# Kernel optimization log

Measured on AMD Instinct MI355X. Metric: run time of the kernel, lower is better.

Reference implementation:

```python
import jax, jax.numpy as jnp
import numpy as np

TEMPERATURE = 0.1
SIGMA = 1.0
NUM_CLASSES = 4
INF = 1e8
EPS = 1e-12


def _l2_normalize(x):
    n = jnp.sqrt(jnp.sum(x * x, axis=-1, keepdims=True))
    return x / jnp.maximum(n, EPS)


def _rbf_kernel(y, gamma):
    # y: [M, P] -> [M, M] exp(-gamma * ||yi - yj||^2)
    sq = jnp.sum(y * y, axis=-1)
    d2 = sq[:, None] + sq[None, :] - 2.0 * (y @ y.T)
    d2 = jnp.maximum(d2, 0.0)
    return jnp.exp(-gamma * d2)


def setup_inputs() -> dict:
    key = jax.random.key(0)
    k1, k2, k3, k4 = jax.random.split(key, 4)
    N, D = 2048, 512
    return {
        "z_i": jax.random.normal(k1, (N, D), dtype=jnp.float32),
        "z_j": jax.random.normal(k2, (N, D), dtype=jnp.float32),
        "labels": jax.random.randint(k3, (N,), 0, NUM_CLASSES, dtype=jnp.int64),
        "z_pos": jax.random.uniform(k4, (N, 1), dtype=jnp.float32),
    }


def reference(z_i, z_j, labels, z_pos):
    N = z_i.shape[0]
    zi = _l2_normalize(z_i)
    zj = _l2_normalize(z_j)

    eye_n = jnp.eye(N, dtype=zi.dtype)
    sim_zii = (zi @ zi.T) / TEMPERATURE - INF * eye_n
    sim_zjj = (zj @ zj.T) / TEMPERATURE - INF * eye_n
    sim_zij = (zi @ zj.T) / TEMPERATURE

    # label agreement mask over the 2N x 2N augmented batch
    labs = jax.nn.one_hot(labels, NUM_CLASSES, dtype=jnp.float32)
    L = jnp.concatenate([labs, labs], axis=0)          # [2N, C]
    eye_2n = jnp.eye(2 * N, dtype=jnp.float32)
    mask = (L @ L.T) * (1.0 - eye_2n)

    # RBF kernel weights over positional labels (detached in original)
    all_pos = jnp.tile(z_pos.reshape(N, -1), (2, 1))   # [2N, P]
    gamma = 1.0 / (2.0 * SIGMA ** 2)
    weights = _rbf_kernel(all_pos, gamma) * (1.0 - eye_2n)

    final_weights = weights * mask
    # NB: torch broadcasting divides column j by rowsum[j]; matrix is symmetric
    final_weights = final_weights / final_weights.sum(axis=1)

    top = jnp.concatenate([sim_zii, sim_zij], axis=1)
    bot = jnp.concatenate([sim_zij.T, sim_zjj], axis=1)
    sim_Z = jnp.concatenate([top, bot], axis=0)        # [2N, 2N]

    log_sim_Z = jax.nn.log_softmax(sim_Z, axis=1)
    loss = (-1.0 / N) * jnp.sum(log_sim_Z * final_weights)
    return loss
```

## Files before the change

kernel.cpp:

```cpp
#include <hip/hip_runtime.h>
#include <hip/hip_bf16.h>

#define D 512
#define INV_T 10.0f
#define INF_VAL 1e8f

#define BM 128
#define BN 128
#define BK 64
#define KSTEPS (D / BK)
#define NTB 32
#define NBLK (NTB * (NTB + 1) / 2)
#define NCHUNK 64

typedef short bf16x8 __attribute__((ext_vector_type(8)));
typedef float f32x4 __attribute__((ext_vector_type(4)));

typedef __attribute__((address_space(3))) unsigned int lds_uint;
typedef __attribute__((address_space(1))) unsigned int gbl_uint;

__device__ __forceinline__ void async_copy16(const ushort* gsrc, ushort* ldst) {
  __builtin_amdgcn_global_load_lds((const gbl_uint*)gsrc, (lds_uint*)ldst, 16, 0, 0);
}

__device__ inline float wave_reduce_sum(float v) {
#pragma unroll
  for (int off = 32; off > 0; off >>= 1) v += __shfl_xor(v, off);
  return v;
}

__device__ __forceinline__ ushort f2bf(float x) {
  __hip_bfloat16 h = __float2bfloat16(x);
  return *reinterpret_cast<ushort*>(&h);
}

__global__ __launch_bounds__(256) void k_prep(const float* __restrict__ zi,
                                              const float* __restrict__ zj,
                                              ushort* __restrict__ zb,
                                              const int* __restrict__ labels,
                                              const float* __restrict__ zpos,
                                              float* __restrict__ sinv, int N) {
  int b = blockIdx.x;
  if (b < 1024) {
    int wv = threadIdx.x >> 6, lane = threadIdx.x & 63;
    int row = b * 4 + wv;
    const float* src = (row < N) ? (zi + (size_t)row * D) : (zj + (size_t)(row - N) * D);
    const float4* s4 = reinterpret_cast<const float4*>(src);
    float4 v0 = s4[lane];
    float4 v1 = s4[lane + 64];
    float ss = 0.f;
    ss = fmaf(v0.x, v0.x, ss); ss = fmaf(v0.y, v0.y, ss);
    ss = fmaf(v0.z, v0.z, ss); ss = fmaf(v0.w, v0.w, ss);
    ss = fmaf(v1.x, v1.x, ss); ss = fmaf(v1.y, v1.y, ss);
    ss = fmaf(v1.z, v1.z, ss); ss = fmaf(v1.w, v1.w, ss);
    ss = wave_reduce_sum(ss);
    float sc = 1.0f / fmaxf(sqrtf(ss), 1e-12f);
    ushort4 o0 = {f2bf(v0.x * sc), f2bf(v0.y * sc), f2bf(v0.z * sc), f2bf(v0.w * sc)};
    ushort4 o1 = {f2bf(v1.x * sc), f2bf(v1.y * sc), f2bf(v1.z * sc), f2bf(v1.w * sc)};
    ushort4* dst = reinterpret_cast<ushort4*>(zb + (size_t)row * D);
    dst[lane] = o0;
    dst[lane + 64] = o1;
  } else {
    __shared__ float scratch[4];
    int j = b - 1024;
    int lj = labels[j];
    float pj = zpos[j];
    float s = 0.f;
    for (int i = threadIdx.x; i < N; i += 256) {
      if (labels[i] == lj) {
        float d = zpos[i] - pj;
        s += __expf(-0.5f * d * d);
      }
    }
    s = wave_reduce_sum(s);
    int lane = threadIdx.x & 63, wv = threadIdx.x >> 6;
    if (lane == 0) scratch[wv] = s;
    __syncthreads();
    if (threadIdx.x == 0) {
      float t = scratch[0] + scratch[1] + scratch[2] + scratch[3];
      sinv[j] = 1.0f / (2.0f * t - 1.0f);
    }
  }
}

__global__ __launch_bounds__(256) void k_tt(const int* __restrict__ labels,
                                            const float* __restrict__ zpos,
                                            const float* __restrict__ sinv,
                                            float* __restrict__ tt, int N) {
  __shared__ float scratch[4];
  int i = blockIdx.x;
  int li = labels[i];
  float pi = zpos[i];
  float s = 0.f;
  for (int j = threadIdx.x; j < N; j += 256) {
    if (labels[j] == li) {
      float d = zpos[j] - pi;
      s += __expf(-0.5f * d * d) * sinv[j];
    }
  }
  s = wave_reduce_sum(s);
  int lane = threadIdx.x & 63, wv = threadIdx.x >> 6;
  if (lane == 0) scratch[wv] = s;
  __syncthreads();
  if (threadIdx.x == 0) {
    tt[i] = scratch[0] + scratch[1] + scratch[2] + scratch[3];
  }
}

__global__ __launch_bounds__(256, 2) void k_gemm(
    const ushort* __restrict__ zb, const int* __restrict__ labels,
    const float* __restrict__ zpos, const float* __restrict__ sinv,
    float* __restrict__ s_ws, float* __restrict__ c_ws, int N) {
  __shared__ __align__(16) ushort sT[2][2][BM * BK];

  const int tid = threadIdx.x;
  const int lane = tid & 63;
  const int wv = tid >> 6;
  const int wr = wv >> 1;
  const int wc = wv & 1;
  const int colq = lane & 15;
  const int laneg = lane >> 4;
  const int twoN = 2 * N;

  const int bid = blockIdx.x;
  int L = (bid & 7) * (NBLK / 8) + (bid >> 3);
  int u = L, rt = 0;
  while (u >= NTB - rt) { u -= NTB - rt; ++rt; }
  const int ct = rt + u;
  const bool diag = (rt == ct);
  const int rowBase = rt * BM;
  const int colBase = ct * BN;

  const int srow = lane >> 3;
  const int sslot = (lane & 7) ^ srow;

  f32x4 acc[4][4] = {};

  {
#pragma unroll
    for (int q = 0; q < 4; ++q) {
      int rloc = wv * 32 + q * 8;
      async_copy16(zb + (size_t)(rowBase + rloc + srow) * D + 0 * BK + sslot * 8,
                   (ushort*)sT[0][0] + rloc * BK);
      if (!diag)
        async_copy16(zb + (size_t)(colBase + rloc + srow) * D + 0 * BK + sslot * 8,
                     (ushort*)sT[0][1] + rloc * BK);
    }
  }
  __syncthreads();

  int cur = 0;
#pragma unroll
  for (int kt = 0; kt < KSTEPS; ++kt) {
    if (kt + 1 < KSTEPS) {
#pragma unroll
      for (int q = 0; q < 4; ++q) {
        int rloc = wv * 32 + q * 8;
        async_copy16(zb + (size_t)(rowBase + rloc + srow) * D + (kt + 1) * BK + sslot * 8,
                     (ushort*)sT[cur ^ 1][0] + rloc * BK);
        if (!diag)
          async_copy16(zb + (size_t)(colBase + rloc + srow) * D + (kt + 1) * BK + sslot * 8,
                       (ushort*)sT[cur ^ 1][1] + rloc * BK);
      }
    }

    const char* Ab = reinterpret_cast<const char*>(sT[cur][0]);
    const char* Bb = diag ? Ab : reinterpret_cast<const char*>(sT[cur][1]);
#pragma unroll
    for (int kk = 0; kk < 2; ++kk) {
      bf16x8 a[4], b[4];
      const int slot = kk * 4 + laneg;
#pragma unroll
      for (int rf = 0; rf < 4; ++rf) {
        int r = wr * 64 + rf * 16 + colq;
        a[rf] = *reinterpret_cast<const bf16x8*>(Ab + r * 128 + (slot ^ (r & 7)) * 16);
      }
#pragma unroll
      for (int cf = 0; cf < 4; ++cf) {
        int c = wc * 64 + cf * 16 + colq;
        b[cf] = *reinterpret_cast<const bf16x8*>(Bb + c * 128 + (slot ^ (c & 7)) * 16);
      }
#pragma unroll
      for (int rf = 0; rf < 4; ++rf)
#pragma unroll
        for (int cf = 0; cf < 4; ++cf)
          acc[rf][cf] = __builtin_amdgcn_mfma_f32_16x16x32_bf16(a[rf], b[cf], acc[rf][cf], 0, 0, 0);
    }

    if (kt + 1 < KSTEPS) {
      __syncthreads();
      cur ^= 1;
    }
  }

  const int wRowBase = rowBase + wr * 64;
  const int wColBase = colBase + wc * 64;
  const int rmodBase = (wRowBase >= N) ? wRowBase - N : wRowBase;
  const int cmodBase = (wColBase >= N) ? wColBase - N : wColBase;

  float rpos[16], rsinv[16];
  unsigned rlab = 0;
#pragma unroll
  for (int rf = 0; rf < 4; ++rf)
#pragma unroll
    for (int rg = 0; rg < 4; ++rg) {
      int idx = rf * 4 + rg;
      int r = rmodBase + rf * 16 + laneg * 4 + rg;
      rpos[idx] = zpos[r];
      rsinv[idx] = sinv[r];
      rlab |= ((unsigned)labels[r] & 3u) << (idx * 2);
    }

  float s_p[16], c_p[16], sc_p[4], cc_p[4];
#pragma unroll
  for (int i = 0; i < 16; ++i) { s_p[i] = 0.f; c_p[i] = 0.f; }

#pragma unroll
  for (int cf = 0; cf < 4; ++cf) {
    int jc = cmodBase + cf * 16 + colq;
    int lc = labels[jc];
    float pc = zpos[jc];
    float si = sinv[jc];
    int col = wColBase + cf * 16 + colq;
    float scf = 0.f, ccf = 0.f;
#pragma unroll
    for (int rf = 0; rf < 4; ++rf)
#pragma unroll
      for (int rg = 0; rg < 4; ++rg) {
        int idx = rf * 4 + rg;
        int row = wRowBase + rf * 16 + laneg * 4 + rg;
        float sim = acc[rf][cf][rg] * INV_T;
        bool dg = (row == col);
        if (dg) sim = -INF_VAL;
        float e = __expf(sim - 10.f);
        s_p[idx] += e;
        scf += e;
        int lr = (int)((rlab >> (idx * 2)) & 3u);
        if (lr == lc && !dg) {
          float d = rpos[idx] - pc;
          float w = __expf(-0.5f * d * d);
          c_p[idx] = fmaf(w * si, sim, c_p[idx]);
          ccf = fmaf(w * rsinv[idx], sim, ccf);
        }
      }
    sc_p[cf] = scf;
    cc_p[cf] = ccf;
  }

#pragma unroll
  for (int idx = 0; idx < 16; ++idx) {
#pragma unroll
    for (int off = 1; off < 16; off <<= 1) {
      s_p[idx] += __shfl_xor(s_p[idx], off);
      c_p[idx] += __shfl_xor(c_p[idx], off);
    }
  }
  if (colq == 0) {
    int cc = ct * 2 + wc;
#pragma unroll
    for (int rf = 0; rf < 4; ++rf)
#pragma unroll
      for (int rg = 0; rg < 4; ++rg) {
        int idx = rf * 4 + rg;
        int row = wRowBase + rf * 16 + laneg * 4 + rg;
        s_ws[(size_t)cc * twoN + row] = s_p[idx];
        c_ws[(size_t)cc * twoN + row] = c_p[idx];
      }
  }

  if (!diag) {
#pragma unroll
    for (int cf = 0; cf < 4; ++cf) {
      sc_p[cf] += __shfl_xor(sc_p[cf], 16);
      sc_p[cf] += __shfl_xor(sc_p[cf], 32);
      cc_p[cf] += __shfl_xor(cc_p[cf], 16);
      cc_p[cf] += __shfl_xor(cc_p[cf], 32);
    }
    if (laneg == 0) {
      int cct = rt * 2 + wr;
#pragma unroll
      for (int cf = 0; cf < 4; ++cf) {
        int rowt = wColBase + cf * 16 + colq;
        s_ws[(size_t)cct * twoN + rowt] = sc_p[cf];
        c_ws[(size_t)cct * twoN + rowt] = cc_p[cf];
      }
    }
  }
}

__global__ __launch_bounds__(256) void k_combine(const float* __restrict__ s_ws,
                                                 const float* __restrict__ c_ws,
                                                 const float* __restrict__ sinv,
                                                 const float* __restrict__ tt,
                                                 float* __restrict__ partial, int N) {
  int a = blockIdx.x * 256 + threadIdx.x;
  int twoN = 2 * N;
  if (a >= twoN) return;
  float s = 0.f, c = 0.f;
  for (int cc = 0; cc < NCHUNK; ++cc) {
    s += s_ws[(size_t)cc * twoN + a];
    c += c_ws[(size_t)cc * twoN + a];
  }
  int ir = (a >= N) ? a - N : a;
  float lse = 10.f + logf(s);
  float wsum = 2.f * tt[ir] - sinv[ir];
  partial[a] = c - wsum * lse;
}

__global__ __launch_bounds__(256) void k_final(const float* __restrict__ partial,
                                               float* __restrict__ out, int N) {
  __shared__ float scratch[4];
  float s = 0.f;
  for (int a = threadIdx.x; a < 2 * N; a += 256) s += partial[a];
  s = wave_reduce_sum(s);
  int lane = threadIdx.x & 63, wv = threadIdx.x >> 6;
  if (lane == 0) scratch[wv] = s;
  __syncthreads();
  if (threadIdx.x == 0) {
    float t = scratch[0] + scratch[1] + scratch[2] + scratch[3];
    out[0] = (-1.0f / (float)N) * t;
  }
}

extern "C" void kernel_launch(void* const* d_in, const int* in_sizes, int n_in,
                              void* d_out, int out_size, void* d_ws, size_t ws_size,
                              hipStream_t stream) {
  (void)n_in; (void)out_size; (void)ws_size;
  const float* zi = (const float*)d_in[0];
  const float* zj = (const float*)d_in[1];
  const int* labels = (const int*)d_in[2];
  const float* zpos = (const float*)d_in[3];
  float* out = (float*)d_out;

  const int N = in_sizes[2];
  const int twoN = 2 * N;

  char* wsb = (char*)d_ws;
  ushort* zb = (ushort*)wsb;
  float* sinv = (float*)(wsb + (size_t)twoN * D * 2);
  float* tt = sinv + N;
  float* s_ws = tt + N;
  float* c_ws = s_ws + (size_t)NCHUNK * twoN;
  float* partial = c_ws + (size_t)NCHUNK * twoN;

  k_prep<<<1024 + 2048, 256, 0, stream>>>(zi, zj, zb, labels, zpos, sinv, N);
  k_tt<<<N, 256, 0, stream>>>(labels, zpos, sinv, tt, N);
  k_gemm<<<NBLK, 256, 0, stream>>>(zb, labels, zpos, sinv, s_ws, c_ws, N);
  k_combine<<<(twoN + 255) / 256, 256, 0, stream>>>(s_ws, c_ws, sinv, tt, partial, N);
  k_final<<<1, 256, 0, stream>>>(partial, out, N);
}
```

Before: 56.72 us.

## Fuse tt computation into GEMM launch and block-reduce in combine

Removes the separate k_tt launch by appending extra blocks to the GEMM grid that compute tt with 16 threads per row, cutting one kernel launch and letting tt run concurrently with the GEMM tiles. k_combine now splits the 64-chunk reduction across 4 waves per 64 rows and reduces each block's partial loss so k_final sums only 64 values. This saves launch overhead and the serial final reduction, but the tt blocks share the GEMM's LDS declaration and launch bounds, and their sequential per-thread loops may tail behind the GEMM blocks.

```diff
diff --git a/kernel.cpp b/kernel.cpp
--- a/kernel.cpp
+++ b/kernel.cpp
@@ -6,11 +6,11 @@
 #define INF_VAL 1e8f
 
 #define BM 128
-#define BN 128
 #define BK 64
 #define KSTEPS (D / BK)
 #define NTB 32
 #define NBLK (NTB * (NTB + 1) / 2)
+#define TTBLK 128
 #define NCHUNK 64
 
 typedef short bf16x8 __attribute__((ext_vector_type(8)));
@@ -83,69 +83,64 @@
   }
 }
 
-__global__ __launch_bounds__(256) void k_tt(const int* __restrict__ labels,
-                                            const float* __restrict__ zpos,
-                                            const float* __restrict__ sinv,
-                                            float* __restrict__ tt, int N) {
-  __shared__ float scratch[4];
-  int i = blockIdx.x;
-  int li = labels[i];
-  float pi = zpos[i];
-  float s = 0.f;
-  for (int j = threadIdx.x; j < N; j += 256) {
-    if (labels[j] == li) {
-      float d = zpos[j] - pi;
-      s += __expf(-0.5f * d * d) * sinv[j];
-    }
-  }
-  s = wave_reduce_sum(s);
-  int lane = threadIdx.x & 63, wv = threadIdx.x >> 6;
-  if (lane == 0) scratch[wv] = s;
-  __syncthreads();
-  if (threadIdx.x == 0) {
-    tt[i] = scratch[0] + scratch[1] + scratch[2] + scratch[3];
-  }
-}
-
 __global__ __launch_bounds__(256, 2) void k_gemm(
     const ushort* __restrict__ zb, const int* __restrict__ labels,
     const float* __restrict__ zpos, const float* __restrict__ sinv,
+    float* __restrict__ tt,
     float* __restrict__ s_ws, float* __restrict__ c_ws, int N) {
+  const int tid = threadIdx.x;
+  const int bid = blockIdx.x;
+  const int twoN = 2 * N;
+
+  if (bid >= NBLK) {
+    int i = (bid - NBLK) * 16 + (tid >> 4);
+    int part = tid & 15;
+    int li = labels[i];
+    float pi = zpos[i];
+    int seg = N >> 4;
+    float s = 0.f;
+    for (int j = part * seg; j < (part + 1) * seg; ++j) {
+      if (labels[j] == li) {
+        float d = zpos[j] - pi;
+        s += __expf(-0.5f * d * d) * sinv[j];
+      }
+    }
+    s += __shfl_xor(s, 1); s += __shfl_xor(s, 2);
+    s += __shfl_xor(s, 4); s += __shfl_xor(s, 8);
+    if (part == 0) tt[i] = s;
+    return;
+  }
+
   __shared__ __align__(16) ushort sT[2][2][BM * BK];
 
-  const int tid = threadIdx.x;
   const int lane = tid & 63;
   const int wv = tid >> 6;
   const int wr = wv >> 1;
   const int wc = wv & 1;
   const int colq = lane & 15;
   const int laneg = lane >> 4;
-  const int twoN = 2 * N;
-
-  const int bid = blockIdx.x;
+
   int L = (bid & 7) * (NBLK / 8) + (bid >> 3);
   int u = L, rt = 0;
   while (u >= NTB - rt) { u -= NTB - rt; ++rt; }
   const int ct = rt + u;
   const bool diag = (rt == ct);
   const int rowBase = rt * BM;
-  const int colBase = ct * BN;
+  const int colBase = ct * BM;
 
   const int srow = lane >> 3;
   const int sslot = (lane & 7) ^ srow;
 
   f32x4 acc[4][4] = {};
 
-  {
-#pragma unroll
-    for (int q = 0; q < 4; ++q) {
-      int rloc = wv * 32 + q * 8;
-      async_copy16(zb + (size_t)(rowBase + rloc + srow) * D + 0 * BK + sslot * 8,
-                   (ushort*)sT[0][0] + rloc * BK);
-      if (!diag)
-        async_copy16(zb + (size_t)(colBase + rloc + srow) * D + 0 * BK + sslot * 8,
-                     (ushort*)sT[0][1] + rloc * BK);
-    }
+#pragma unroll
+  for (int q = 0; q < 4; ++q) {
+    int rloc = wv * 32 + q * 8;
+    async_copy16(zb + (size_t)(rowBase + rloc + srow) * D + 0 * BK + sslot * 8,
+                 (ushort*)sT[0][0] + rloc * BK);
+    if (!diag)
+      async_copy16(zb + (size_t)(colBase + rloc + srow) * D + 0 * BK + sslot * 8,
+                   (ushort*)sT[0][1] + rloc * BK);
   }
   __syncthreads();
 
@@ -256,15 +251,15 @@
     }
   }
   if (colq == 0) {
-    int cc = ct * 2 + wc;
+    int m = ct * 2 + wc;
 #pragma unroll
     for (int rf = 0; rf < 4; ++rf)
 #pragma unroll
       for (int rg = 0; rg < 4; ++rg) {
         int idx = rf * 4 + rg;
         int row = wRowBase + rf * 16 + laneg * 4 + rg;
-        s_ws[(size_t)cc * twoN + row] = s_p[idx];
-        c_ws[(size_t)cc * twoN + row] = c_p[idx];
+        s_ws[(size_t)m * twoN + row] = s_p[idx];
+        c_ws[(size_t)m * twoN + row] = c_p[idx];
       }
   }
 
@@ -277,12 +272,12 @@
       cc_p[cf] += __shfl_xor(cc_p[cf], 32);
     }
     if (laneg == 0) {
-      int cct = rt * 2 + wr;
+      int m = rt * 2 + wr;
 #pragma unroll
       for (int cf = 0; cf < 4; ++cf) {
         int rowt = wColBase + cf * 16 + colq;
-        s_ws[(size_t)cct * twoN + rowt] = sc_p[cf];
-        c_ws[(size_t)cct * twoN + rowt] = cc_p[cf];
+        s_ws[(size_t)m * twoN + rowt] = sc_p[cf];
+        c_ws[(size_t)m * twoN + rowt] = cc_p[cf];
       }
     }
   }
@@ -292,34 +287,39 @@
                                                  const float* __restrict__ c_ws,
                                                  const float* __restrict__ sinv,
                                                  const float* __restrict__ tt,
-                                                 float* __restrict__ partial, int N) {
-  int a = blockIdx.x * 256 + threadIdx.x;
+                                                 float* __restrict__ bsum, int N) {
+  __shared__ float sS[4][64], sC[4][64];
+  int b = blockIdx.x, t = threadIdx.x;
+  int r = t & 63, g = t >> 6;
   int twoN = 2 * N;
-  if (a >= twoN) return;
+  int a = b * 64 + r;
   float s = 0.f, c = 0.f;
-  for (int cc = 0; cc < NCHUNK; ++cc) {
-    s += s_ws[(size_t)cc * twoN + a];
-    c += c_ws[(size_t)cc * twoN + a];
-  }
-  int ir = (a >= N) ? a - N : a;
-  float lse = 10.f + logf(s);
-  float wsum = 2.f * tt[ir] - sinv[ir];
-  partial[a] = c - wsum * lse;
-}
-
-__global__ __launch_bounds__(256) void k_final(const float* __restrict__ partial,
-                                               float* __restrict__ out, int N) {
-  __shared__ float scratch[4];
-  float s = 0.f;
-  for (int a = threadIdx.x; a < 2 * N; a += 256) s += partial[a];
+  for (int k = 0; k < NCHUNK / 4; ++k) {
+    int m = g * (NCHUNK / 4) + k;
+    s += s_ws[(size_t)m * twoN + a];
+    c += c_ws[(size_t)m * twoN + a];
+  }
+  sS[g][r] = s;
+  sC[g][r] = c;
+  __syncthreads();
+  if (t < 64) {
+    float st = sS[0][t] + sS[1][t] + sS[2][t] + sS[3][t];
+    float ct = sC[0][t] + sC[1][t] + sC[2][t] + sC[3][t];
+    int aa = b * 64 + t;
+    int ir = (aa >= N) ? aa - N : aa;
+    float lse = 10.f + logf(st);
+    float wsum = 2.f * tt[ir] - sinv[ir];
+    float p = ct - wsum * lse;
+    p = wave_reduce_sum(p);
+    if (t == 0) bsum[b] = p;
+  }
+}
+
+__global__ __launch_bounds__(64) void k_final(const float* __restrict__ bsum,
+                                              float* __restrict__ out, int N) {
+  float s = bsum[threadIdx.x];
   s = wave_reduce_sum(s);
-  int lane = threadIdx.x & 63, wv = threadIdx.x >> 6;
-  if (lane == 0) scratch[wv] = s;
-  __syncthreads();
-  if (threadIdx.x == 0) {
-    float t = scratch[0] + scratch[1] + scratch[2] + scratch[3];
-    out[0] = (-1.0f / (float)N) * t;
-  }
+  if (threadIdx.x == 0) out[0] = (-1.0f / (float)N) * s;
 }
 
 extern "C" void kernel_launch(void* const* d_in, const int* in_sizes, int n_in,
@@ -341,11 +341,10 @@
   float* tt = sinv + N;
   float* s_ws = tt + N;
   float* c_ws = s_ws + (size_t)NCHUNK * twoN;
-  float* partial = c_ws + (size_t)NCHUNK * twoN;
+  float* bsum = c_ws + (size_t)NCHUNK * twoN;
 
   k_prep<<<1024 + 2048, 256, 0, stream>>>(zi, zj, zb, labels, zpos, sinv, N);
-  k_tt<<<N, 256, 0, stream>>>(labels, zpos, sinv, tt, N);
-  k_gemm<<<NBLK, 256, 0, stream>>>(zb, labels, zpos, sinv, s_ws, c_ws, N);
-  k_combine<<<(twoN + 255) / 256, 256, 0, stream>>>(s_ws, c_ws, sinv, tt, partial, N);
-  k_final<<<1, 256, 0, stream>>>(partial, out, N);
-}
+  k_gemm<<<NBLK + TTBLK, 256, 0, stream>>>(zb, labels, zpos, sinv, tt, s_ws, c_ws, N);
+  k_combine<<<twoN / 64, 256, 0, stream>>>(s_ws, c_ws, sinv, tt, bsum, N);
+  k_final<<<1, 64, 0, stream>>>(bsum, out, N);
+}
```

Result: slower. 60.14 us (+6.0%).
